# Kernel tuning notes

Measured on AMD Instinct MI355X. Metric: run time of the kernel, lower is better.

The kernel has to match this reference:

```python
import jax, jax.numpy as jnp
import numpy as np

EPS = 1e-5

def _conv1(x, W):
    # 1x1 conv: W [Cout, Cin], x [B, Cin, H, W]
    return jnp.einsum('oi,bihw->bohw', W, x)

def _bn(x, p):
    # p: [4, C] rows = (gamma, beta, running_mean, running_var); inference-mode BN
    g, b, m, v = p[0], p[1], p[2], p[3]
    s = (1, -1, 1, 1)
    return (x - m.reshape(s)) * (g.reshape(s) * jax.lax.rsqrt(v.reshape(s) + EPS)) + b.reshape(s)

def _block(x, W1, p1, W2, p2):
    # Conv1x1 -> BN -> ReLU -> Conv1x1 -> BN -> ReLU  (Composition / Decomposition conv block)
    h = jax.nn.relu(_bn(_conv1(x, W1), p1))
    return jax.nn.relu(_bn(_conv1(h, W2), p2))

def _gru(h, x, Wg, bg, Wc, bc):
    # ConvGRU cell with 1x1 kernels: h is prev hidden, x is message input
    g = jax.nn.sigmoid(_conv1(jnp.concatenate([x, h], axis=1), Wg) + bg.reshape(1, -1, 1, 1))
    r, u = jnp.split(g, 2, axis=1)  # reset, update gates
    c = jnp.tanh(_conv1(jnp.concatenate([x, r * h], axis=1), Wc) + bc.reshape(1, -1, 1, 1))
    return (1.0 - u) * h + u * c


def setup_inputs() -> dict:
    key = jax.random.key(0)
    B, HD, H, W = 8, 10, 192, 192
    ks = iter(jax.random.split(key, 64))
    def nrm(shape, s=1.0):
        return s * jax.random.normal(next(ks), shape, dtype=jnp.float32)
    def att(shape):
        return jax.random.uniform(next(ks), shape, dtype=jnp.float32)
    def bnp(C):
        return jnp.stack([
            jax.random.uniform(next(ks), (C,), minval=0.5, maxval=1.5, dtype=jnp.float32),
            0.1 * jax.random.normal(next(ks), (C,), dtype=jnp.float32),
            0.1 * jax.random.normal(next(ks), (C,), dtype=jnp.float32),
            jax.random.uniform(next(ks), (C,), minval=0.5, maxval=1.5, dtype=jnp.float32)])
    inp = dict(
        xf=nrm((B, HD, H, W)),
        xh=nrm((2, B, HD, H, W)),
        xp=nrm((6, B, HD, H, W)),
        h_att=att((3, B, 1, H, W)),
        p_att=att((7, B, 1, H, W)),
        dW1=nrm((2 * HD, 2 * HD), 0.2), dbn1=bnp(2 * HD), dW2=nrm((HD, 2 * HD), 0.2), dbn2=bnp(HD),
        uW1=nrm((2 * HD, 2 * HD), 0.2), ubn1=bnp(2 * HD), uW2=nrm((HD, 2 * HD), 0.2), ubn2=bnp(HD),
        lW1=nrm((2 * HD, 2 * HD), 0.2), lbn1=bnp(2 * HD), lW2=nrm((HD, 2 * HD), 0.2), lbn2=bnp(HD),
        guWg=nrm((2 * HD, 2 * HD), 0.2), gubg=nrm((2 * HD,), 0.1),
        guWc=nrm((HD, 2 * HD), 0.2), gubc=nrm((HD,), 0.1),
        glWg=nrm((2 * HD, 2 * HD), 0.2), glbg=nrm((2 * HD,), 0.1),
        glWc=nrm((HD, 2 * HD), 0.2), glbc=nrm((HD,), 0.1),
    )
    return inp


def reference(xf, xh, xp, h_att, p_att,
              dW1, dbn1, dW2, dbn2,
              uW1, ubn1, uW2, ubn2,
              lW1, lbn1, lW2, lbn2,
              guWg, gubg, guWc, gubc,
              glWg, glbg, glWc, glbc):
    # Decomposition: conv_fh(cat(xf * h_att[i+1], xh[i])) for the two halves
    decomp_u = _block(jnp.concatenate([xf * h_att[1], xh[0]], axis=1), dW1, dbn1, dW2, dbn2)
    decomp_l = _block(jnp.concatenate([xf * h_att[2], xh[1]], axis=1), dW1, dbn1, dW2, dbn2)
    # Composition upper: parts 1..4 -> xp[0..3], attention maps p_att[1..4]
    com_att_u = p_att[1] + p_att[2] + p_att[3] + p_att[4]
    comp_u = sum(_block(jnp.concatenate([xh[0], xp[i] * com_att_u], axis=1), uW1, ubn1, uW2, ubn2)
                 for i in range(4))
    xh_u = _gru(xh[0], decomp_u + comp_u, guWg, gubg, guWc, gubc)
    # Composition lower: parts 5..6 -> xp[4..5], attention maps p_att[5..6]
    com_att_l = p_att[5] + p_att[6]
    comp_l = sum(_block(jnp.concatenate([xh[1], xp[i] * com_att_l], axis=1), lW1, lbn1, lW2, lbn2)
                 for i in (4, 5))
    xh_l = _gru(xh[1], decomp_l + comp_l, glWg, glbg, glWc, glbc)
    return jnp.stack([xh_u, xh_l])  # [2, B, hidden, H, W]
```

## Files before the change

### kernel.cpp

```cpp
#include <hip/hip_runtime.h>

#define HD 10
#define C2 20
#define PIX (192*192)
#define NB 8
#define NPIX (NB*PIX)
#define CHW (NB*HD*PIX)
#define EPSB 1e-5f
#define BPB (PIX/256)

__device__ __forceinline__ float sigm(float x) {
    return __builtin_amdgcn_rcpf(1.0f + __expf(-x));
}
__device__ __forceinline__ float tanh_fast(float x) {
    return 1.0f - 2.0f * __builtin_amdgcn_rcpf(1.0f + __expf(2.0f * x));
}

__global__ __launch_bounds__(256) void half_kernel(
    const float* __restrict__ xf, const float* __restrict__ xh, const float* __restrict__ xp,
    const float* __restrict__ h_att, const float* __restrict__ p_att,
    const float* __restrict__ dW1, const float* __restrict__ dbn1,
    const float* __restrict__ dW2, const float* __restrict__ dbn2,
    const float* __restrict__ uW1, const float* __restrict__ ubn1,
    const float* __restrict__ uW2, const float* __restrict__ ubn2,
    const float* __restrict__ lW1, const float* __restrict__ lbn1,
    const float* __restrict__ lW2, const float* __restrict__ lbn2,
    const float* __restrict__ guWg, const float* __restrict__ gubg,
    const float* __restrict__ guWc, const float* __restrict__ gubc,
    const float* __restrict__ glWg, const float* __restrict__ glbg,
    const float* __restrict__ glWc, const float* __restrict__ glbc,
    float* __restrict__ out)
{
    const int bid  = blockIdx.x;
    const int half = bid & 1;
    const int bx   = bid >> 1;
    const int b    = bx / BPB;
    const int s    = (bx - b * BPB) * 256 + threadIdx.x;
    const int base  = b * (HD*PIX) + s;
    const int abase = b * PIX + s;

    const float* Wc1  = half ? lW1  : uW1;
    const float* cbn1 = half ? lbn1 : ubn1;
    const float* Wc2  = half ? lW2  : uW2;
    const float* cbn2 = half ? lbn2 : ubn2;
    const float* Wg = half ? glWg : guWg;
    const float* bg = half ? glbg : gubg;
    const float* Wc = half ? glWc : guWc;
    const float* bc = half ? glbc : gubc;

    const float* xhh = xh + half * CHW;
    float* outh = out + half * CHW;

    float vxh[HD];
    #pragma unroll
    for (int c = 0; c < HD; ++c) vxh[c] = xhh[base + c*PIX];

    const float ha = h_att[(1 + half) * NPIX + abase];
    float catt = 0.f;
    {
        const int mstart = half ? 5 : 1;
        const int natt   = half ? 2 : 4;
        #pragma unroll
        for (int j = 0; j < 4; ++j)
            if (j < natt) catt += p_att[(mstart + j) * NPIX + abase];
    }

    float m[HD];
    {
        float in[C2];
        #pragma unroll
        for (int c = 0; c < HD; ++c) { in[c] = xf[base + c*PIX] * ha; in[HD + c] = vxh[c]; }
        float h[C2];
        #pragma unroll
        for (int o = 0; o < C2; ++o) {
            float a = 0.f;
            #pragma unroll
            for (int k = 0; k < C2; ++k) a = fmaf(dW1[o*C2 + k], in[k], a);
            float sc = dbn1[o] * rsqrtf(dbn1[3*C2 + o] + EPSB);
            float tr = dbn1[C2 + o] - sc * dbn1[2*C2 + o];
            h[o] = fmaxf(fmaf(a, sc, tr), 0.f);
        }
        #pragma unroll
        for (int o = 0; o < HD; ++o) {
            float a = 0.f;
            #pragma unroll
            for (int k = 0; k < C2; ++k) a = fmaf(dW2[o*C2 + k], h[k], a);
            float sc = dbn2[o] * rsqrtf(dbn2[3*HD + o] + EPSB);
            float tr = dbn2[HD + o] - sc * dbn2[2*HD + o];
            m[o] = fmaxf(fmaf(a, sc, tr), 0.f);
        }
    }

    {
        float s1[C2], s2[HD], t2[HD];
        #pragma unroll
        for (int o = 0; o < C2; ++o)
            s1[o] = cbn1[o] * rsqrtf(cbn1[3*C2 + o] + EPSB);
        #pragma unroll
        for (int o = 0; o < HD; ++o) {
            s2[o] = cbn2[o] * rsqrtf(cbn2[3*HD + o] + EPSB);
            t2[o] = cbn2[HD + o] - s2[o] * cbn2[2*HD + o];
        }
        float pre[C2];
        #pragma unroll
        for (int o = 0; o < C2; ++o) {
            float a = 0.f;
            #pragma unroll
            for (int k = 0; k < HD; ++k) a = fmaf(Wc1[o*C2 + k], vxh[k], a);
            float t1 = cbn1[C2 + o] - s1[o] * cbn1[2*C2 + o];
            pre[o] = fmaf(a, s1[o], t1);
        }
        const int pstart = half ? 4 : 0;
        const int nparts = half ? 2 : 4;
        #pragma unroll
        for (int i = 0; i < 4; ++i) {
            if (i < nparts) {
                float xpi[HD];
                #pragma unroll
                for (int c = 0; c < HD; ++c)
                    xpi[c] = xp[(pstart + i) * CHW + base + c*PIX] * catt;
                float h[C2];
                #pragma unroll
                for (int o = 0; o < C2; ++o) {
                    float a = 0.f;
                    #pragma unroll
                    for (int k = 0; k < HD; ++k) a = fmaf(Wc1[o*C2 + HD + k], xpi[k], a);
                    h[o] = fmaxf(fmaf(a, s1[o], pre[o]), 0.f);
                }
                #pragma unroll
                for (int o = 0; o < HD; ++o) {
                    float a = 0.f;
                    #pragma unroll
                    for (int k = 0; k < C2; ++k) a = fmaf(Wc2[o*C2 + k], h[k], a);
                    m[o] += fmaxf(fmaf(a, s2[o], t2[o]), 0.f);
                }
            }
        }
    }

    float g[C2];
    #pragma unroll
    for (int o = 0; o < C2; ++o) {
        float a = bg[o];
        #pragma unroll
        for (int k = 0; k < HD; ++k) a = fmaf(Wg[o*C2 + k], m[k], a);
        #pragma unroll
        for (int k = 0; k < HD; ++k) a = fmaf(Wg[o*C2 + HD + k], vxh[k], a);
        g[o] = sigm(a);
    }
    float rh[HD];
    #pragma unroll
    for (int k = 0; k < HD; ++k) rh[k] = g[k] * vxh[k];
    #pragma unroll
    for (int o = 0; o < HD; ++o) {
        float a = bc[o];
        #pragma unroll
        for (int k = 0; k < HD; ++k) a = fmaf(Wc[o*C2 + k], m[k], a);
        #pragma unroll
        for (int k = 0; k < HD; ++k) a = fmaf(Wc[o*C2 + HD + k], rh[k], a);
        float c = tanh_fast(a);
        float u = g[HD + o];
        outh[base + o*PIX] = fmaf(u, c - vxh[o], vxh[o]);
    }
}

extern "C" void kernel_launch(void* const* d_in, const int* in_sizes, int n_in,
                              void* d_out, int out_size, void* d_ws, size_t ws_size,
                              hipStream_t stream) {
    const float* xf    = (const float*)d_in[0];
    const float* xh    = (const float*)d_in[1];
    const float* xp    = (const float*)d_in[2];
    const float* h_att = (const float*)d_in[3];
    const float* p_att = (const float*)d_in[4];
    const float* dW1   = (const float*)d_in[5];
    const float* dbn1  = (const float*)d_in[6];
    const float* dW2   = (const float*)d_in[7];
    const float* dbn2  = (const float*)d_in[8];
    const float* uW1   = (const float*)d_in[9];
    const float* ubn1  = (const float*)d_in[10];
    const float* uW2   = (const float*)d_in[11];
    const float* ubn2  = (const float*)d_in[12];
    const float* lW1   = (const float*)d_in[13];
    const float* lbn1  = (const float*)d_in[14];
    const float* lW2   = (const float*)d_in[15];
    const float* lbn2  = (const float*)d_in[16];
    const float* guWg  = (const float*)d_in[17];
    const float* gubg  = (const float*)d_in[18];
    const float* guWc  = (const float*)d_in[19];
    const float* gubc  = (const float*)d_in[20];
    const float* glWg  = (const float*)d_in[21];
    const float* glbg  = (const float*)d_in[22];
    const float* glWc  = (const float*)d_in[23];
    const float* glbc  = (const float*)d_in[24];

    dim3 grid((NPIX / 256) * 2), block(256);
    half_kernel<<<grid, block, 0, stream>>>(
        xf, xh, xp, h_att, p_att,
        dW1, dbn1, dW2, dbn2,
        uW1, ubn1, uW2, ubn2,
        lW1, lbn1, lW2, lbn2,
        guWg, gubg, guWc, gubc,
        glWg, glbg, glWc, glbc,
        (float*)d_out);
}
```

Measured before the change: 94.39 us.

## Double-buffer xp part loads ahead of compute and set min-blocks launch bound

```diff
diff --git a/kernel.cpp b/kernel.cpp
--- a/kernel.cpp
+++ b/kernel.cpp
@@ -16,7 +16,7 @@
     return 1.0f - 2.0f * __builtin_amdgcn_rcpf(1.0f + __expf(2.0f * x));
 }
 
-__global__ __launch_bounds__(256) void half_kernel(
+__global__ __launch_bounds__(256, 3) void half_kernel(
     const float* __restrict__ xf, const float* __restrict__ xh, const float* __restrict__ xp,
     const float* __restrict__ h_att, const float* __restrict__ p_att,
     const float* __restrict__ dW1, const float* __restrict__ dbn1,
@@ -51,6 +51,16 @@
     const float* xhh = xh + half * CHW;
     float* outh = out + half * CHW;
 
+    const int pstart = half ? 4 : 0;
+    const int nparts = half ? 2 : 4;
+
+#define LOAD_XP(BUF, PI)                                        \
+    do {                                                        \
+        _Pragma("unroll")                                       \
+        for (int c = 0; c < HD; ++c)                            \
+            BUF[c] = xp[(PI) * CHW + base + c*PIX];             \
+    } while (0)
+
     float vxh[HD];
     #pragma unroll
     for (int c = 0; c < HD; ++c) vxh[c] = xhh[base + c*PIX];
@@ -64,6 +74,9 @@
         for (int j = 0; j < 4; ++j)
             if (j < natt) catt += p_att[(mstart + j) * NPIX + abase];
     }
+
+    float xpA[HD], xpB[HD];
+    LOAD_XP(xpA, pstart + 0);
 
     float m[HD];
     {
@@ -110,32 +123,42 @@
             float t1 = cbn1[C2 + o] - s1[o] * cbn1[2*C2 + o];
             pre[o] = fmaf(a, s1[o], t1);
         }
-        const int pstart = half ? 4 : 0;
-        const int nparts = half ? 2 : 4;
-        #pragma unroll
-        for (int i = 0; i < 4; ++i) {
-            if (i < nparts) {
-                float xpi[HD];
-                #pragma unroll
-                for (int c = 0; c < HD; ++c)
-                    xpi[c] = xp[(pstart + i) * CHW + base + c*PIX] * catt;
-                float h[C2];
-                #pragma unroll
-                for (int o = 0; o < C2; ++o) {
-                    float a = 0.f;
-                    #pragma unroll
-                    for (int k = 0; k < HD; ++k) a = fmaf(Wc1[o*C2 + HD + k], xpi[k], a);
-                    h[o] = fmaxf(fmaf(a, s1[o], pre[o]), 0.f);
-                }
-                #pragma unroll
-                for (int o = 0; o < HD; ++o) {
-                    float a = 0.f;
-                    #pragma unroll
-                    for (int k = 0; k < C2; ++k) a = fmaf(Wc2[o*C2 + k], h[k], a);
-                    m[o] += fmaxf(fmaf(a, s2[o], t2[o]), 0.f);
-                }
-            }
-        }
+
+#define COMP_PART(BUF)                                                      \
+    do {                                                                    \
+        _Pragma("unroll")                                                   \
+        for (int c = 0; c < HD; ++c) BUF[c] *= catt;                        \
+        float hcb[C2];                                                      \
+        _Pragma("unroll")                                                   \
+        for (int o = 0; o < C2; ++o) {                                      \
+            float a = 0.f;                                                  \
+            _Pragma("unroll")                                               \
+            for (int k = 0; k < HD; ++k)                                    \
+                a = fmaf(Wc1[o*C2 + HD + k], BUF[k], a);                    \
+            hcb[o] = fmaxf(fmaf(a, s1[o], pre[o]), 0.f);                    \
+        }                                                                   \
+        _Pragma("unroll")                                                   \
+        for (int o = 0; o < HD; ++o) {                                      \
+            float a = 0.f;                                                  \
+            _Pragma("unroll")                                               \
+            for (int k = 0; k < C2; ++k)                                    \
+                a = fmaf(Wc2[o*C2 + k], hcb[k], a);                         \
+            m[o] += fmaxf(fmaf(a, s2[o], t2[o]), 0.f);                      \
+        }                                                                   \
+    } while (0)
+
+        LOAD_XP(xpB, pstart + 1);
+        COMP_PART(xpA);
+        if (nparts > 2) {
+            LOAD_XP(xpA, pstart + 2);
+            COMP_PART(xpB);
+            LOAD_XP(xpB, pstart + 3);
+            COMP_PART(xpA);
+            COMP_PART(xpB);
+        } else {
+            COMP_PART(xpB);
+        }
+#undef COMP_PART
     }
 
     float g[C2];
@@ -162,6 +185,7 @@
         float u = g[HD + o];
         outh[base + o*PIX] = fmaf(u, c - vxh[o], vxh[o]);
     }
+#undef LOAD_XP
 }
 
 extern "C" void kernel_launch(void* const* d_in, const int* in_sizes, int n_in,
```

New measurement: 120.1 us. +27.3%, slower.
